# Optimization experiments

Measured on AMD Instinct MI355X. Metric: run time of the kernel, lower is better.

The kernel has to match this reference:

```python
import jax, jax.numpy as jnp
import numpy as np

TOTAL_DIM = 64  # 16+16+16+8+8
HIDDEN = 4 * TOTAL_DIM
NUM_HEADS = 8


def _fourier(x, num_freqs):
    # Dyadic Fourier features: sin/cos of 2^j * x for j in [0, num_freqs).
    # Output dim = input_dim * num_freqs * 2 (matches embed_dim in the module).
    freqs = 2.0 ** jnp.arange(num_freqs, dtype=x.dtype)  # (F,)
    phase = x[..., :, None] * freqs                       # (..., in, F)
    out = jnp.concatenate([jnp.sin(phase), jnp.cos(phase)], axis=-1)  # (..., in, 2F)
    return out.reshape(x.shape[:-1] + (-1,))


def setup_inputs() -> dict:
    key = jax.random.key(0)
    k1, k2, k3, k4, k5, k6 = jax.random.split(key, 6)
    B, Nq, Nk, D = 8, 256, 256, 10
    query_states = jax.random.normal(k1, (B, Nq, D), dtype=jnp.float32)
    key_states = jax.random.normal(k2, (B, Nk, D), dtype=jnp.float32)
    W1 = jax.random.normal(k3, (TOTAL_DIM, HIDDEN), dtype=jnp.float32) / np.sqrt(TOTAL_DIM)
    b1 = jnp.zeros((HIDDEN,), dtype=jnp.float32)
    W2 = jax.random.normal(k4, (HIDDEN, NUM_HEADS), dtype=jnp.float32) / np.sqrt(HIDDEN)
    b2 = jnp.zeros((NUM_HEADS,), dtype=jnp.float32)
    return {"query_states": query_states, "key_states": key_states,
            "W1": W1, "b1": b1, "W2": W2, "b2": b2}


def _features(query_states, key_states):
    # Slice per-ship fields, then broadcast pairwise: q -> (B,Nq,1,*), k -> (B,1,Nk,*)
    q_team = query_states[:, :, None, 0]          # (B,Nq,1)
    k_team = key_states[:, None, :, 0]            # (B,1,Nk)
    q_pos = query_states[:, :, None, 3:5]
    k_pos = key_states[:, None, :, 3:5]
    q_vel = query_states[:, :, None, 5:7]
    k_vel = key_states[:, None, :, 5:7]
    q_att = query_states[:, :, None, 7:9]
    k_att = key_states[:, None, :, 7:9]

    delta_pos = k_pos - q_pos                     # (B,Nq,Nk,2)
    delta_vel = k_vel - q_vel                     # (B,Nq,Nk,2)
    feat_delta_input = jnp.concatenate([delta_pos, delta_vel], axis=-1)  # (B,Nq,Nk,4)

    dist_sq = jnp.sum(delta_pos ** 2, axis=-1, keepdims=True)
    dist = jnp.sqrt(dist_sq + 1e-6)
    inv_dist = 1.0 / (dist + 0.1)
    feat_dist_input = jnp.concatenate([dist, inv_dist], axis=-1)         # (B,Nq,Nk,2)

    bearing = delta_pos / (dist + 1e-6)
    ata = jnp.sum(bearing * q_att, axis=-1, keepdims=True)
    aspect = jnp.sum(bearing * k_att, axis=-1, keepdims=True)
    feat_angle_input = jnp.concatenate([ata, aspect], axis=-1)           # (B,Nq,Nk,2)

    dot_dp_dv = jnp.sum(delta_pos * delta_vel, axis=-1, keepdims=True)
    speed_sq = jnp.sum(delta_vel ** 2, axis=-1, keepdims=True)
    ttca = jnp.tanh(jax.nn.relu(-dot_dp_dv / (speed_sq + 1e-6)))
    feat_intercept_input = jnp.concatenate([ttca, dist], axis=-1)        # (B,Nq,Nk,2)

    same_team = (q_team == k_team).astype(query_states.dtype)[..., None]
    q_speed = jnp.linalg.norm(q_vel, axis=-1, keepdims=True)
    k_speed = jnp.linalg.norm(k_vel, axis=-1, keepdims=True)
    delta_speed = k_speed - q_speed
    feat_team_input = jnp.concatenate([same_team, delta_speed], axis=-1)  # (B,Nq,Nk,2)

    out_dist = _fourier(feat_dist_input, 4)        # 16
    out_angle = _fourier(feat_angle_input, 4)      # 16
    out_delta = _fourier(feat_delta_input, 2)      # 16
    out_intercept = _fourier(feat_intercept_input, 2)  # 8
    out_team = _fourier(feat_team_input, 2)        # 8
    return jnp.concatenate([out_dist, out_angle, out_delta, out_intercept, out_team], axis=-1)


def reference(query_states, key_states, W1, b1, W2, b2):
    combined = _features(query_states, key_states)          # (B,Nq,Nk,64)
    h = jax.nn.silu(combined @ W1 + b1)                     # (B,Nq,Nk,256)
    bias = h @ W2 + b2                                      # (B,Nq,Nk,H)
    return jnp.transpose(bias, (0, 3, 1, 2))                # (B,H,Nq,Nk)
```

## Files before the change

kernel.cpp:

```cpp
#include <hip/hip_runtime.h>
#include <math.h>

#define NB 8
#define NQ 256
#define NK 256
#define DIN 10
#define FDIM 64
#define HIDDEN 256
#define NH 8
#define ROWS_PER_BLK 4

#define FSTRIDE 64
#define HSTRIDE 264

typedef float f32x4 __attribute__((ext_vector_type(4)));
typedef short bf16x8 __attribute__((ext_vector_type(8)));

__device__ __forceinline__ short f2bf(float f) {
    return (short)((__float_as_uint(f) + 0x8000u) >> 16);
}
__device__ __forceinline__ unsigned pack2(float a, float b) {
    unsigned ua = __float_as_uint(a) + 0x8000u;
    unsigned ub = __float_as_uint(b) + 0x8000u;
    return __builtin_amdgcn_perm(ub, ua, 0x07060302);
}

__device__ __forceinline__ void four4(float x, float* dst) {
    float s1 = __sinf(x), c1 = __cosf(x);
    float s2 = 2.f * s1 * c1, c2 = 1.f - 2.f * s1 * s1;
    float s4 = 2.f * s2 * c2, c4 = 1.f - 2.f * s2 * s2;
    float s8 = 2.f * s4 * c4, c8 = 1.f - 2.f * s4 * s4;
    dst[0] = s1; dst[1] = s2; dst[2] = s4; dst[3] = s8;
    dst[4] = c1; dst[5] = c2; dst[6] = c4; dst[7] = c8;
}
__device__ __forceinline__ void four2(float x, float* dst) {
    float s1 = __sinf(x), c1 = __cosf(x);
    dst[0] = s1; dst[1] = 2.f * s1 * c1;
    dst[2] = c1; dst[3] = 1.f - 2.f * s1 * s1;
}

__global__ __launch_bounds__(256, 2) void relfeat_mfma_kernel(
    const float* __restrict__ q, const float* __restrict__ k,
    const float* __restrict__ W1, const float* __restrict__ b1,
    const float* __restrict__ W2, const float* __restrict__ b2,
    float* __restrict__ out)
{
    __shared__ __align__(16) short feat_s[NK * FSTRIDE];
    __shared__ __align__(16) short h_s[2 * 32 * HSTRIDE];

    const int t = threadIdx.x;
    const int wave = t >> 6;
    const int l15 = t & 15;
    const int quad = (t >> 4) & 3;
    const int b = blockIdx.x >> 6;
    const int i0 = (blockIdx.x & 63) * ROWS_PER_BLK;
    const int swr = l15 & 7;

    const float* kp = k + ((size_t)b * NK + t) * DIN;
    const float k0 = kp[0], k3 = kp[3], k4 = kp[4], k5 = kp[5], k6 = kp[6],
                k7 = kp[7], k8 = kp[8];

    bf16x8 w2f[8];
#pragma unroll
    for (int k2 = 0; k2 < 8; ++k2) {
        bf16x8 v;
#pragma unroll
        for (int e = 0; e < 8; ++e)
            v[e] = f2bf(-0.69314718f *
                        W2[(size_t)(k2 * 32 + quad * 8 + e) * NH + (l15 & 7)]);
        w2f[k2] = v;
    }
    const float b2v = (l15 < NH) ? b2[l15] : 0.f;

    const int n0 = wave * 64;
    bf16x8 w1f[4][2];
#pragma unroll
    for (int nt = 0; nt < 4; ++nt)
#pragma unroll
        for (int ks = 0; ks < 2; ++ks) {
            const float* wp = W1 + (size_t)(ks * 32 + quad * 8) * HIDDEN
                              + (n0 + nt * 16 + l15);
            bf16x8 v;
#pragma unroll
            for (int e = 0; e < 8; ++e)
                v[e] = f2bf(-1.44269504f * wp[(size_t)e * HIDDEN]);
            w1f[nt][ks] = v;
        }
    float4 b1q[4];
#pragma unroll
    for (int nt = 0; nt < 4; ++nt) {
        float4 bb = *(const float4*)&b1[n0 + nt * 16 + quad * 4];
        b1q[nt] = make_float4(-1.44269504f * bb.x, -1.44269504f * bb.y,
                              -1.44269504f * bb.z, -1.44269504f * bb.w);
    }

#pragma unroll 1
    for (int row = 0; row < ROWS_PER_BLK; ++row) {
        const int i = i0 + row;

        {
            const float* qp = q + ((size_t)b * NQ + i) * DIN;
            const float q0 = qp[0], q3 = qp[3], q4 = qp[4], q5 = qp[5],
                        q6 = qp[6], q7 = qp[7], q8 = qp[8];

            const float dpx = k3 - q3, dpy = k4 - q4;
            const float dvx = k5 - q5, dvy = k6 - q6;
            const float dist = sqrtf(dpx * dpx + dpy * dpy + 1e-6f);
            const float inv_dist = 1.0f / (dist + 0.1f);
            const float inv_d2 = 1.0f / (dist + 1e-6f);
            const float bear_x = dpx * inv_d2, bear_y = dpy * inv_d2;
            const float ata = bear_x * q7 + bear_y * q8;
            const float aspect = bear_x * k7 + bear_y * k8;
            const float dot_dp_dv = dpx * dvx + dpy * dvy;
            const float speed_sq = dvx * dvx + dvy * dvy;
            const float ttca = tanhf(fmaxf(0.f, -dot_dp_dv / (speed_sq + 1e-6f)));
            const float same_team = (q0 == k0) ? 1.f : 0.f;
            const float q_speed = sqrtf(q5 * q5 + q6 * q6);
            const float k_speed = sqrtf(k5 * k5 + k6 * k6);
            const float delta_speed = k_speed - q_speed;

            float feat[FDIM];
            four4(dist,        feat + 0);
            four4(inv_dist,    feat + 8);
            four4(ata,         feat + 16);
            four4(aspect,      feat + 24);
            four2(dpx,         feat + 32);
            four2(dpy,         feat + 36);
            four2(dvx,         feat + 40);
            four2(dvy,         feat + 44);
            four2(ttca,        feat + 48);
            four2(dist,        feat + 52);
            four2(same_team,   feat + 56);
            four2(delta_speed, feat + 60);

            const int sw = t & 7;
#pragma unroll
            for (int c8 = 0; c8 < 8; ++c8) {
                uint4 v;
                v.x = pack2(feat[c8 * 8 + 0], feat[c8 * 8 + 1]);
                v.y = pack2(feat[c8 * 8 + 2], feat[c8 * 8 + 3]);
                v.z = pack2(feat[c8 * 8 + 4], feat[c8 * 8 + 5]);
                v.w = pack2(feat[c8 * 8 + 6], feat[c8 * 8 + 7]);
                *(uint4*)&feat_s[t * FSTRIDE + ((c8 ^ sw) * 8)] = v;
            }
        }
        __syncthreads();

#pragma unroll 1
        for (int hc = 0; hc < 8; ++hc) {
            const int p0 = hc * 32;
            short* hb = &h_s[(hc & 1) * 32 * HSTRIDE];

            f32x4 acc[4][2];
#pragma unroll
            for (int nt = 0; nt < 4; ++nt)
#pragma unroll
                for (int mt = 0; mt < 2; ++mt)
                    acc[nt][mt] = (f32x4){b1q[nt].x, b1q[nt].y, b1q[nt].z, b1q[nt].w};
#pragma unroll
            for (int ks = 0; ks < 2; ++ks)
#pragma unroll
                for (int mt = 0; mt < 2; ++mt) {
                    const int r2 = p0 + mt * 16 + l15;
                    const bf16x8 fb = *(const bf16x8*)
                        &feat_s[r2 * FSTRIDE + (((ks * 4 + quad) ^ swr) * 8)];
#pragma unroll
                    for (int nt = 0; nt < 4; ++nt)
                        acc[nt][mt] = __builtin_amdgcn_mfma_f32_16x16x32_bf16(
                            w1f[nt][ks], fb, acc[nt][mt], 0, 0, 0);
                }

#pragma unroll
            for (int nt = 0; nt < 4; ++nt)
#pragma unroll
                for (int mt = 0; mt < 2; ++mt) {
                    const int pair = mt * 16 + l15;
                    const int hbase = n0 + nt * 16 + quad * 4;
                    float s[4];
#pragma unroll
                    for (int r = 0; r < 4; ++r) {
                        const float a = acc[nt][mt][r];
                        const float e = __builtin_amdgcn_exp2f(a);
                        s[r] = a * __builtin_amdgcn_rcpf(1.f + e);
                    }
                    uint2 pk;
                    pk.x = pack2(s[0], s[1]);
                    pk.y = pack2(s[2], s[3]);
                    *(uint2*)&hb[pair * HSTRIDE + hbase] = pk;
                }
            __syncthreads();

            if ((wave >> 1) == (hc & 1)) {
                const int pw = (wave & 1) * 16;
                f32x4 acc2 = (f32x4){b2v, b2v, b2v, b2v};
#pragma unroll
                for (int k2 = 0; k2 < 8; ++k2) {
                    const bf16x8 ha = *(const bf16x8*)
                        &hb[(pw + l15) * HSTRIDE + k2 * 32 + quad * 8];
                    acc2 = __builtin_amdgcn_mfma_f32_16x16x32_bf16(
                        ha, w2f[k2], acc2, 0, 0, 0);
                }
                if (l15 < NH) {
                    float* op = out + (((size_t)b * NH + l15) * NQ + i) * NK
                                + (p0 + pw + quad * 4);
                    *(float4*)op = make_float4(acc2[0], acc2[1], acc2[2], acc2[3]);
                }
            }
        }
    }
}

extern "C" void kernel_launch(void* const* d_in, const int* in_sizes, int n_in,
                              void* d_out, int out_size, void* d_ws, size_t ws_size,
                              hipStream_t stream) {
    const float* q  = (const float*)d_in[0];
    const float* k  = (const float*)d_in[1];
    const float* W1 = (const float*)d_in[2];
    const float* b1 = (const float*)d_in[3];
    const float* W2 = (const float*)d_in[4];
    const float* b2 = (const float*)d_in[5];
    float* out = (float*)d_out;

    dim3 grid(NB * NQ / ROWS_PER_BLK);
    dim3 block(NK);
    relfeat_mfma_kernel<<<grid, block, 0, stream>>>(q, k, W1, b1, W2, b2, out);
}
```

Measured before the change: 115.4 us.

## Process 64 key pairs per chunk with single h buffer and all-wave second GEMM

```diff
diff --git a/kernel.cpp b/kernel.cpp
--- a/kernel.cpp
+++ b/kernel.cpp
@@ -1,4 +1,5 @@
 #include <hip/hip_runtime.h>
+#include <hip/hip_bf16.h>
 #include <math.h>
 
 #define NB 8
@@ -19,10 +20,11 @@
 __device__ __forceinline__ short f2bf(float f) {
     return (short)((__float_as_uint(f) + 0x8000u) >> 16);
 }
-__device__ __forceinline__ unsigned pack2(float a, float b) {
-    unsigned ua = __float_as_uint(a) + 0x8000u;
-    unsigned ub = __float_as_uint(b) + 0x8000u;
-    return __builtin_amdgcn_perm(ub, ua, 0x07060302);
+__device__ __forceinline__ unsigned pk2(float a, float b) {
+    __hip_bfloat162 h = __float22bfloat162_rn(make_float2(a, b));
+    unsigned u;
+    __builtin_memcpy(&u, &h, sizeof(u));
+    return u;
 }
 
 __device__ __forceinline__ void four4(float x, float* dst) {
@@ -46,7 +48,7 @@
     float* __restrict__ out)
 {
     __shared__ __align__(16) short feat_s[NK * FSTRIDE];
-    __shared__ __align__(16) short h_s[2 * 32 * HSTRIDE];
+    __shared__ __align__(16) short h_s[64 * HSTRIDE];
 
     const int t = threadIdx.x;
     const int wave = t >> 6;
@@ -137,30 +139,29 @@
 #pragma unroll
             for (int c8 = 0; c8 < 8; ++c8) {
                 uint4 v;
-                v.x = pack2(feat[c8 * 8 + 0], feat[c8 * 8 + 1]);
-                v.y = pack2(feat[c8 * 8 + 2], feat[c8 * 8 + 3]);
-                v.z = pack2(feat[c8 * 8 + 4], feat[c8 * 8 + 5]);
-                v.w = pack2(feat[c8 * 8 + 6], feat[c8 * 8 + 7]);
+                v.x = pk2(feat[c8 * 8 + 0], feat[c8 * 8 + 1]);
+                v.y = pk2(feat[c8 * 8 + 2], feat[c8 * 8 + 3]);
+                v.z = pk2(feat[c8 * 8 + 4], feat[c8 * 8 + 5]);
+                v.w = pk2(feat[c8 * 8 + 6], feat[c8 * 8 + 7]);
                 *(uint4*)&feat_s[t * FSTRIDE + ((c8 ^ sw) * 8)] = v;
             }
         }
         __syncthreads();
 
 #pragma unroll 1
-        for (int hc = 0; hc < 8; ++hc) {
-            const int p0 = hc * 32;
-            short* hb = &h_s[(hc & 1) * 32 * HSTRIDE];
-
-            f32x4 acc[4][2];
+        for (int c = 0; c < 4; ++c) {
+            const int p0 = c * 64;
+
+            f32x4 acc[4][4];
 #pragma unroll
             for (int nt = 0; nt < 4; ++nt)
 #pragma unroll
-                for (int mt = 0; mt < 2; ++mt)
+                for (int mt = 0; mt < 4; ++mt)
                     acc[nt][mt] = (f32x4){b1q[nt].x, b1q[nt].y, b1q[nt].z, b1q[nt].w};
 #pragma unroll
             for (int ks = 0; ks < 2; ++ks)
 #pragma unroll
-                for (int mt = 0; mt < 2; ++mt) {
+                for (int mt = 0; mt < 4; ++mt) {
                     const int r2 = p0 + mt * 16 + l15;
                     const bf16x8 fb = *(const bf16x8*)
                         &feat_s[r2 * FSTRIDE + (((ks * 4 + quad) ^ swr) * 8)];
@@ -170,10 +171,12 @@
                             w1f[nt][ks], fb, acc[nt][mt], 0, 0, 0);
                 }
 
+            __syncthreads();
+
 #pragma unroll
             for (int nt = 0; nt < 4; ++nt)
 #pragma unroll
-                for (int mt = 0; mt < 2; ++mt) {
+                for (int mt = 0; mt < 4; ++mt) {
                     const int pair = mt * 16 + l15;
                     const int hbase = n0 + nt * 16 + quad * 4;
                     float s[4];
@@ -184,19 +187,19 @@
                         s[r] = a * __builtin_amdgcn_rcpf(1.f + e);
                     }
                     uint2 pk;
-                    pk.x = pack2(s[0], s[1]);
-                    pk.y = pack2(s[2], s[3]);
-                    *(uint2*)&hb[pair * HSTRIDE + hbase] = pk;
+                    pk.x = pk2(s[0], s[1]);
+                    pk.y = pk2(s[2], s[3]);
+                    *(uint2*)&h_s[pair * HSTRIDE + hbase] = pk;
                 }
             __syncthreads();
 
-            if ((wave >> 1) == (hc & 1)) {
-                const int pw = (wave & 1) * 16;
+            {
+                const int pw = wave * 16;
                 f32x4 acc2 = (f32x4){b2v, b2v, b2v, b2v};
 #pragma unroll
                 for (int k2 = 0; k2 < 8; ++k2) {
-                    const bf16x8 ha = *(const bf16x8*)
-                        &hb[(pw + l15) * HSTRIDE + k2 * 32 + quad * 8];
+                    const bf16x8 ha = *(const bf16x8*)&h_s[(pw + l15) * HSTRIDE
+                                                            + k2 * 32 + quad * 8];
                     acc2 = __builtin_amdgcn_mfma_f32_16x16x32_bf16(
                         ha, w2f[k2], acc2, 0, 0, 0);
                 }
```

Result: no change. 117.0 us (+1.5%).
